# Performance work log

Measured on AMD Instinct MI355X. Metric: run time of the kernel, lower is better.

The kernel has to match this reference:

```python
import jax, jax.numpy as jnp
import numpy as np

B, S, HID = 2, 2048, 4096
NH, NKV, D = 32, 8, 128
GROUPS = NH // NKV  # 4 query heads per KV head
THETA = 10000.0
MAX_SEQ = 4096


def _rope_tables():
    half = D // 2
    inv_freq = 1.0 / (THETA ** (np.arange(half, dtype=np.float32) / half))
    t = np.arange(MAX_SEQ, dtype=np.float32)
    freqs = np.outer(t, inv_freq)  # [MAX_SEQ, D//2]
    return jnp.asarray(np.cos(freqs)), jnp.asarray(np.sin(freqs))

ROPE_COS, ROPE_SIN = _rope_tables()


def _apply_rope(x, cos, sin):
    # x: [B, S, H, D]; cos/sin: [S, D//2]; half-split (NeoX) rotation as in _apply_rope_inline
    half = x.shape[-1] // 2
    x0, x1 = x[..., :half], x[..., half:]
    c = cos[None, :, None, :]
    s = sin[None, :, None, :]
    return jnp.concatenate([x0 * c - x1 * s, x0 * s + x1 * c], axis=-1)


def setup_inputs() -> dict:
    key = jax.random.key(0)
    ks = jax.random.split(key, 5)
    wscale = 1.0 / np.sqrt(HID).astype(np.float32)  # keep activations O(1)
    return {
        "x": jax.random.normal(ks[0], (B, S, HID), dtype=jnp.float32),
        "positions": jnp.arange(S, dtype=jnp.int32),
        "w_q": jax.random.normal(ks[1], (NH * D, HID), dtype=jnp.float32) * wscale,
        "w_k": jax.random.normal(ks[2], (NKV * D, HID), dtype=jnp.float32) * wscale,
        "w_v": jax.random.normal(ks[3], (NKV * D, HID), dtype=jnp.float32) * wscale,
        "w_o": jax.random.normal(ks[4], (HID, NH * D), dtype=jnp.float32) * wscale,
    }


def reference(x, positions, w_q, w_k, w_v, w_o):
    cos = ROPE_COS[positions]  # [S, D//2]
    sin = ROPE_SIN[positions]
    # Separate Q/K/V projections (no bias), as in the training forward()
    q = (x @ w_q.T).reshape(B, S, NH, D)
    k = (x @ w_k.T).reshape(B, S, NKV, D)
    v = (x @ w_v.T).reshape(B, S, NKV, D)
    q = _apply_rope(q, cos, sin)
    k = _apply_rope(k, cos, sin)
    # [B, H, S, D] layout
    q = q.transpose(0, 2, 1, 3)
    k = k.transpose(0, 2, 1, 3)
    v = v.transpose(0, 2, 1, 3)
    # GQA: group query heads over shared KV heads instead of repeating K/V
    qg = q.reshape(B, NKV, GROUPS, S, D)
    scale = 1.0 / jnp.sqrt(jnp.float32(D))
    scores = jnp.einsum("bkgqd,bkmd->bkgqm", qg, k) * scale  # [B, NKV, G, Sq, Skv]
    causal = jnp.tril(jnp.ones((S, S), dtype=bool))
    scores = jnp.where(causal[None, None, None], scores, jnp.float32(-jnp.inf))
    probs = jax.nn.softmax(scores, axis=-1)
    ctx = jnp.einsum("bkgqm,bkmd->bkgqd", probs, v)  # [B, NKV, G, S, D]
    ctx = ctx.reshape(B, NH, S, D).transpose(0, 2, 1, 3).reshape(B, S, NH * D)
    return ctx @ w_o.T
```

## Files before the change

### kernel.cpp

```cpp
#include <hip/hip_runtime.h>
#include <math.h>

typedef short s16x8 __attribute__((ext_vector_type(8)));
typedef float f32x4 __attribute__((ext_vector_type(4)));
typedef unsigned u32x4 __attribute__((ext_vector_type(4)));
typedef unsigned short u16;

#define S_LEN 2048
#define HID_DIM 4096
#define NH_Q 32
#define NKV_H 8
#define DHEAD 128

__device__ __forceinline__ u16 f2bf(float f) {
  unsigned u = __builtin_bit_cast(unsigned, f);
  u += 0x7fffu + ((u >> 16) & 1u);
  return (u16)(u >> 16);
}

__device__ __forceinline__ void gload16(const u16* g, u16* l) {
  __builtin_amdgcn_global_load_lds(
      (const __attribute__((address_space(1))) void*)g,
      (__attribute__((address_space(3))) void*)l, 16, 0, 0);
}

__global__ void cvt_kernel(const float* __restrict__ in, u16* __restrict__ out, int n4) {
  int stride = gridDim.x * blockDim.x;
  for (int i = blockIdx.x * blockDim.x + threadIdx.x; i < n4; i += stride) {
    float4 f = ((const float4*)in)[i];
    uint2 o;
    o.x = (unsigned)f2bf(f.x) | ((unsigned)f2bf(f.y) << 16);
    o.y = (unsigned)f2bf(f.z) | ((unsigned)f2bf(f.w) << 16);
    ((uint2*)out)[i] = o;
  }
}

__global__ void cvt_all_kernel(const float* __restrict__ x, const float* __restrict__ wq,
                               const float* __restrict__ wk, const float* __restrict__ wv,
                               const float* __restrict__ wo, u16* __restrict__ x_bf,
                               u16* __restrict__ wqkv_bf, u16* __restrict__ wo_bf,
                               const int* __restrict__ positions, float* __restrict__ cos_t,
                               float* __restrict__ sin_t, int with_wo) {
  const int R0 = 4194304, R1 = 8388608, R2 = 9437184, R3 = 10485760, R4 = 14680064;
  const int cvt_end = with_wo ? R4 : R3;
  const int rope_units = 32768;
  const int total = cvt_end + rope_units;
  const int stride = gridDim.x * blockDim.x;
  for (int i = blockIdx.x * blockDim.x + threadIdx.x; i < total; i += stride) {
    if (i < cvt_end) {
      const float* src;
      u16* dst;
      int off;
      if (i < R0)      { src = x;  dst = x_bf;               off = i; }
      else if (i < R1) { src = wq; dst = wqkv_bf;            off = i - R0; }
      else if (i < R2) { src = wk; dst = wqkv_bf + 16777216; off = i - R1; }
      else if (i < R3) { src = wv; dst = wqkv_bf + 20971520; off = i - R2; }
      else             { src = wo; dst = wo_bf;              off = i - R3; }
      float4 f = ((const float4*)src)[off];
      uint2 o;
      o.x = (unsigned)f2bf(f.x) | ((unsigned)f2bf(f.y) << 16);
      o.y = (unsigned)f2bf(f.z) | ((unsigned)f2bf(f.w) << 16);
      ((uint2*)dst)[off] = o;
    } else {
      int base = (i - cvt_end) * 4;
#pragma unroll
      for (int e = 0; e < 4; ++e) {
        int idx = base + e;
        int s = idx >> 6, j = idx & 63;
        float pos = (float)positions[s];
        float inv = expf(-(float)j * (9.210340371976184f / 64.0f));
        float sv, cv;
        sincosf(pos * inv, &sv, &cv);
        cos_t[idx] = cv;
        sin_t[idx] = sv;
      }
    }
  }
}

__global__ void rope_table_kernel(const int* __restrict__ positions,
                                  float* __restrict__ cos_t, float* __restrict__ sin_t) {
  int idx = blockIdx.x * 256 + threadIdx.x;
  if (idx >= S_LEN * 64) return;
  int s = idx >> 6, j = idx & 63;
  float pos = (float)positions[s];
  float inv = expf(-(float)j * (9.210340371976184f / 64.0f));
  float sv, cv;
  sincosf(pos * inv, &sv, &cv);
  cos_t[idx] = cv;
  sin_t[idx] = sv;
}

template<int EPI>
__global__ __launch_bounds__(512, 2) void gemmp_kernel(
    const u16* __restrict__ A, const u16* __restrict__ B,
    void* __restrict__ outp, int M, int N, int K,
    const float* __restrict__ cos_t, const float* __restrict__ sin_t) {
  __shared__ u16 LDS[73728];
  const int t = threadIdx.x;
  const int wave = t >> 6, lane = t & 63;
  const int l15 = lane & 15, lhi = lane >> 4;
  const int wr = wave >> 2, wc = wave & 3;
  const int gx = gridDim.x;
  const int nwg = gx * gridDim.y;
  const int id = blockIdx.y * gx + blockIdx.x;
  const int swz = (id & 7) * (nwg >> 3) + (id >> 3);
  const int bm = (swz / gx) * 128, bn = (swz % gx) * 256;

  const int sw = l15 & 7;
  int aoff[4][2], boff[2][2];
#pragma unroll
  for (int q = 0; q < 4; ++q)
#pragma unroll
    for (int ks = 0; ks < 2; ++ks)
      aoff[q][ks] = wr * 4096 + (q * 16 + l15) * 64 + (((ks << 2) + lhi) ^ sw) * 8;
#pragma unroll
  for (int f = 0; f < 2; ++f)
#pragma unroll
    for (int ks = 0; ks < 2; ++ks)
      boff[f][ks] = (f * 64 + wc * 16 + l15) * 64 + (((ks << 2) + lhi) ^ sw) * 8;

  const int lr1 = t >> 3;
  const int cs1 = ((t & 7) ^ (lr1 & 7)) * 8;
  const int ldsw = wave * 512;

  const f32x4 fz = {0.f, 0.f, 0.f, 0.f};
  f32x4 acc[4][4];
#pragma unroll
  for (int mf = 0; mf < 4; ++mf)
#pragma unroll
    for (int nf = 0; nf < 4; ++nf) acc[mf][nf] = fz;

  auto stageA = [&](int tile, int buf) {
    const size_t kb = (size_t)tile * 64;
    gload16(A + (size_t)(bm + lr1) * K + kb + cs1, &LDS[buf * 8192 + ldsw]);
    gload16(A + (size_t)(bm + 64 + lr1) * K + kb + cs1, &LDS[buf * 8192 + 4096 + ldsw]);
  };
  auto stageB = [&](int tile, int h, int buf) {
    const size_t kb = (size_t)tile * 64;
    gload16(B + (size_t)(bn + h * 128 + lr1) * K + kb + cs1,
            &LDS[24576 + buf * 16384 + h * 8192 + ldsw]);
    gload16(B + (size_t)(bn + h * 128 + 64 + lr1) * K + kb + cs1,
            &LDS[24576 + buf * 16384 + h * 8192 + 4096 + ldsw]);
  };

  s16x8 afr0[4][2], afr1[4][2];
  s16x8 bfr00[2][2], bfr01[2][2];
  s16x8 bfr10[2][2], bfr11[2][2];

#define READ_TILE(SET, BUF)                                                \
  do {                                                                     \
    const int _b = (BUF);                                                  \
    const int _ba = _b * 8192;                                             \
    _Pragma("unroll") for (int q = 0; q < 4; ++q)                          \
      _Pragma("unroll") for (int ks = 0; ks < 2; ++ks)                     \
        afr##SET[q][ks] = *(const s16x8*)&LDS[_ba + aoff[q][ks]];          \
    const int _b0 = 24576 + _b * 16384;                                    \
    _Pragma("unroll") for (int f = 0; f < 2; ++f)                          \
      _Pragma("unroll") for (int ks = 0; ks < 2; ++ks)                     \
        bfr0##SET[f][ks] = *(const s16x8*)&LDS[_b0 + boff[f][ks]];         \
    const int _b1 = _b0 + 8192;                                            \
    _Pragma("unroll") for (int f = 0; f < 2; ++f)                          \
      _Pragma("unroll") for (int ks = 0; ks < 2; ++ks)                     \
        bfr1##SET[f][ks] = *(const s16x8*)&LDS[_b1 + boff[f][ks]];         \
  } while (0)

#define MFMA_HALF(SET, NFH, BH)                                            \
  do {                                                                     \
    __builtin_amdgcn_s_setprio(1);                                         \
    _Pragma("unroll") for (int q = 0; q < 4; ++q)                          \
      _Pragma("unroll") for (int f = 0; f < 2; ++f)                        \
        _Pragma("unroll") for (int ks = 0; ks < 2; ++ks)                   \
          acc[q][(NFH)*2 + f] = __builtin_amdgcn_mfma_f32_16x16x32_bf16(   \
              afr##SET[q][ks], bfr##BH##SET[f][ks], acc[q][(NFH)*2 + f],   \
              0, 0, 0);                                                    \
    __builtin_amdgcn_s_setprio(0);                                         \
  } while (0)

#define TILE_BODY(SET, OSET, TT)                                           \
  do {                                                                     \
    const int _tt = (TT);                                                  \
    const bool _s2 = _tt + 2 < nt;                                         \
    if (_s2) { stageA(_tt + 2, nx2); stageB(_tt + 2, 0, nx2); }            \
    asm volatile("s_waitcnt lgkmcnt(0)" ::: "memory");                     \
    __builtin_amdgcn_sched_barrier(0);                                     \
    MFMA_HALF(SET, 0, 0);                                                  \
    if (_s2) stageB(_tt + 2, 1, nx2);                                      \
    if (_tt + 1 < nt) {                                                    \
      if (_s2) { asm volatile("s_waitcnt vmcnt(6)" ::: "memory"); }        \
      else     { asm volatile("s_waitcnt vmcnt(0)" ::: "memory"); }        \
      __builtin_amdgcn_sched_barrier(0);                                   \
      __builtin_amdgcn_s_barrier();                                        \
      __builtin_amdgcn_sched_barrier(0);                                   \
      READ_TILE(OSET, nxt1);                                               \
    }                                                                      \
    MFMA_HALF(SET, 1, 1);                                                  \
    nxt1 = nx2;                                                            \
    nx2 = (nx2 == 2) ? 0 : nx2 + 1;                                        \
  } while (0)

  const int nt = K >> 6;
  stageA(0, 0); stageB(0, 0, 0); stageB(0, 1, 0);
  stageA(1, 1); stageB(1, 0, 1); stageB(1, 1, 1);
  asm volatile("s_waitcnt vmcnt(6)" ::: "memory");
  __builtin_amdgcn_sched_barrier(0);
  __builtin_amdgcn_s_barrier();
  __builtin_amdgcn_sched_barrier(0);
  READ_TILE(0, 0);

  int nxt1 = 1, nx2 = 2;
  for (int tt = 0; tt < nt; tt += 2) {
    TILE_BODY(0, 1, tt);
    TILE_BODY(1, 0, tt + 1);
  }
#undef TILE_BODY
#undef MFMA_HALF
#undef READ_TILE

  if constexpr (EPI == 0) {
    float* C = (float*)outp;
#pragma unroll
    for (int mf = 0; mf < 4; ++mf) {
      int rb = bm + wr * 64 + mf * 16 + lhi * 4;
#pragma unroll
      for (int nfi = 0; nfi < 4; ++nfi) {
        int col = bn + wc * 16 + (nfi & 1) * 64 + (nfi >> 1) * 128 + l15;
#pragma unroll
        for (int i = 0; i < 4; ++i) C[(size_t)(rb + i) * N + col] = acc[mf][nfi][i];
      }
    }
  } else {
    u16* qp = (u16*)outp;
    u16* kp = qp + 16777216;
    u16* vp = kp + 4194304;
    if (bn < 5120) {
      const bool isQ = bn < 4096;
      u16* O = isQ ? qp : kp;
      const int hb = isQ ? (bn >> 7) : ((bn - 4096) >> 7);
      const int Hh = isQ ? NH_Q : NKV_H;
      const int j = wc * 16 + l15;
#pragma unroll
      for (int mf = 0; mf < 4; ++mf) {
        int rb = bm + wr * 64 + mf * 16 + lhi * 4;
#pragma unroll
        for (int p = 0; p < 2; ++p) {
          int head = hb + p;
#pragma unroll
          for (int i = 0; i < 4; ++i) {
            int m = rb + i;
            int b = m >> 11, srw = m & 2047;
            float c = cos_t[srw * 64 + j];
            float s = sin_t[srw * 64 + j];
            float x0 = acc[mf][2 * p][i];
            float x1 = acc[mf][2 * p + 1][i];
            size_t base = ((size_t)(b * Hh + head) * S_LEN + srw) * DHEAD;
            O[base + j] = f2bf(x0 * c - x1 * s);
            O[base + j + 64] = f2bf(x0 * s + x1 * c);
          }
        }
      }
    } else {
#pragma unroll
      for (int mf = 0; mf < 4; ++mf) {
        int rb = bm + wr * 64 + mf * 16 + lhi * 4;
#pragma unroll
        for (int nfi = 0; nfi < 4; ++nfi) {
          int colrel = bn - 5120 + wc * 16 + (nfi & 1) * 64 + (nfi >> 1) * 128 + l15;
          int head = colrel >> 7, d = colrel & 127;
#pragma unroll
          for (int i = 0; i < 4; ++i) {
            int m = rb + i;
            int b = m >> 11, srw = m & 2047;
            vp[((size_t)(b * NKV_H + head) * DHEAD + d) * S_LEN + srw] = f2bf(acc[mf][nfi][i]);
          }
        }
      }
    }
  }
}

template<int EPI, bool ABF16, bool BBF16>
__global__ __launch_bounds__(256) void gemm_kernel(
    const void* __restrict__ Aptr, const void* __restrict__ Bptr,
    void* __restrict__ outp, void* __restrict__ outp2, int M, int N, int K,
    const float* __restrict__ cos_t, const float* __restrict__ sin_t, int Hh) {
  __shared__ u16 As[128][72];
  __shared__ u16 Bs[128][72];
  const int t = threadIdx.x;
  const int wave = t >> 6, lane = t & 63;
  const int l15 = lane & 15, lhi = lane >> 4;
  const int gx = gridDim.x;
  const int nwg = gx * gridDim.y;
  const int id = blockIdx.y * gx + blockIdx.x;
  const int swz = (id & 7) * (nwg >> 3) + (id >> 3);
  const int bm = (swz / gx) * 128, bn = (swz % gx) * 128;

  const f32x4 fz = {0.f, 0.f, 0.f, 0.f};
  f32x4 acc[2][8];
#pragma unroll
  for (int a0 = 0; a0 < 2; ++a0)
#pragma unroll
    for (int b0 = 0; b0 < 8; ++b0) acc[a0][b0] = fz;

  for (int kt = 0; kt < K; kt += 64) {
    __syncthreads();
    if (ABF16) {
      const u16* A = (const u16*)Aptr;
#pragma unroll
      for (int p = 0; p < 4; ++p) {
        int row = p * 32 + (t >> 3), kc = (t & 7) * 8;
        *(s16x8*)&As[row][kc] = *(const s16x8*)(A + (size_t)(bm + row) * K + kt + kc);
      }
    } else {
      const float* A = (const float*)Aptr;
#pragma unroll
      for (int p = 0; p < 8; ++p) {
        int row = p * 16 + (t >> 4), kc = (t & 15) * 4;
        float4 f = *(const float4*)(A + (size_t)(bm + row) * K + kt + kc);
        unsigned* dst = (unsigned*)&As[row][kc];
        dst[0] = (unsigned)f2bf(f.x) | ((unsigned)f2bf(f.y) << 16);
        dst[1] = (unsigned)f2bf(f.z) | ((unsigned)f2bf(f.w) << 16);
      }
    }
    if (BBF16) {
      const u16* Bw = (const u16*)Bptr;
#pragma unroll
      for (int p = 0; p < 4; ++p) {
        int row = p * 32 + (t >> 3), kc = (t & 7) * 8;
        *(s16x8*)&Bs[row][kc] = *(const s16x8*)(Bw + (size_t)(bn + row) * K + kt + kc);
      }
    } else {
      const float* Bw = (const float*)Bptr;
#pragma unroll
      for (int p = 0; p < 8; ++p) {
        int row = p * 16 + (t >> 4), kc = (t & 15) * 4;
        float4 f = *(const float4*)(Bw + (size_t)(bn + row) * K + kt + kc);
        unsigned* dst = (unsigned*)&Bs[row][kc];
        dst[0] = (unsigned)f2bf(f.x) | ((unsigned)f2bf(f.y) << 16);
        dst[1] = (unsigned)f2bf(f.z) | ((unsigned)f2bf(f.w) << 16);
      }
    }
    __syncthreads();
#pragma unroll
    for (int ks = 0; ks < 2; ++ks) {
      s16x8 bfr[8];
#pragma unroll
      for (int nf = 0; nf < 8; ++nf)
        bfr[nf] = *(const s16x8*)&Bs[nf * 16 + l15][ks * 32 + lhi * 8];
#pragma unroll
      for (int mf = 0; mf < 2; ++mf) {
        s16x8 a = *(const s16x8*)&As[wave * 32 + mf * 16 + l15][ks * 32 + lhi * 8];
#pragma unroll
        for (int nf = 0; nf < 8; ++nf)
          acc[mf][nf] = __builtin_amdgcn_mfma_f32_16x16x32_bf16(a, bfr[nf], acc[mf][nf], 0, 0, 0);
      }
    }
  }

  if (EPI == 0) {
    float* C = (float*)outp;
#pragma unroll
    for (int mf = 0; mf < 2; ++mf)
#pragma unroll
      for (int nf = 0; nf < 8; ++nf) {
        int col = bn + nf * 16 + l15;
        int rb = bm + wave * 32 + mf * 16 + lhi * 4;
#pragma unroll
        for (int i = 0; i < 4; ++i) C[(size_t)(rb + i) * N + col] = acc[mf][nf][i];
      }
  } else if (EPI == 2) {
    u16* O = (u16*)outp;
    int h = bn >> 7;
#pragma unroll
    for (int mf = 0; mf < 2; ++mf)
#pragma unroll
      for (int nf = 0; nf < 4; ++nf) {
        int j = nf * 16 + l15;
        int rb = bm + wave * 32 + mf * 16 + lhi * 4;
#pragma unroll
        for (int i = 0; i < 4; ++i) {
          int m = rb + i;
          int b = m >> 11, srow = m & 2047;
          float c = cos_t[srow * 64 + j];
          float s = sin_t[srow * 64 + j];
          float x0 = acc[mf][nf][i];
          float x1 = acc[mf][nf + 4][i];
          size_t base = ((size_t)(b * Hh + h) * S_LEN + srow) * DHEAD;
          O[base + j] = f2bf(x0 * c - x1 * s);
          O[base + j + 64] = f2bf(x0 * s + x1 * c);
        }
      }
  } else {
    u16* O = (u16*)outp;
#pragma unroll
    for (int mf = 0; mf < 2; ++mf)
#pragma unroll
      for (int nf = 0; nf < 8; ++nf) {
        int col = bn + nf * 16 + l15;
        int h = col >> 7, d = col & 127;
        int rb = bm + wave * 32 + mf * 16 + lhi * 4;
#pragma unroll
        for (int i = 0; i < 4; ++i) {
          int m = rb + i;
          int b = m >> 11, srow = m & 2047;
          O[((size_t)(b * Hh + h) * DHEAD + d) * S_LEN + srow] = f2bf(acc[mf][nf][i]);
        }
      }
  }
}

#define KIDX(r, c) (((r) * 128 + (c)) ^ (((r) & 7) << 3))
#define VIDX(d, kv) (((d) * 64 + (kv)) ^ (((d) & 7) << 3))
__global__ __launch_bounds__(512) void attn_kernel(
    const u16* __restrict__ q, const u16* __restrict__ k, const u16* __restrict__ vt,
    u16* __restrict__ ctx) {
  __shared__ u16 Ks[64 * 128];
  __shared__ u16 Vts[128 * 64];

  const int t = threadIdx.x;
  const int wave = t >> 6, lane = t & 63;
  const int l15 = lane & 15, lhi = lane >> 4;
  const int pi = blockIdx.x, h = blockIdx.y, b = blockIdx.z;
  const int kvh = h >> 2;
  const int qsub[2] = {pi, 15 - pi};
  const int ntiles = 32 - 2 * pi;

  const u16* qb = q + ((size_t)(b * NH_Q + h)) * S_LEN * DHEAD;
  const u16* kb = k + ((size_t)(b * NKV_H + kvh)) * S_LEN * DHEAD;
  const u16* vtb = vt + ((size_t)(b * NKV_H + kvh)) * DHEAD * S_LEN;

  s16x8 qf[2][4];
#pragma unroll
  for (int s = 0; s < 2; ++s)
#pragma unroll
    for (int ks = 0; ks < 4; ++ks)
      qf[s][ks] = *(const s16x8*)(qb + (size_t)(qsub[s] * 128 + wave * 16 + l15) * DHEAD +
                                  ks * 32 + lhi * 8);

  const f32x4 fz = {0.f, 0.f, 0.f, 0.f};
  f32x4 acc[2][8];
#pragma unroll
  for (int s = 0; s < 2; ++s)
#pragma unroll
    for (int i = 0; i < 8; ++i) acc[s][i] = fz;
  float mrow[2] = {-INFINITY, -INFINITY};
  float lsum[2] = {0.f, 0.f};

  const float scale = 0.08838834764831845f;

  const int sl0 = l15 | (((2 * lhi) & 3) << 4);
  const int sl1 = sl0 | 16;
  const bool hisel = (lhi & 2) != 0;

  const int krow = t >> 3, kd0 = (t & 7) * 16;
  const int vrow = t >> 2, vk0 = (t & 3) * 16;
  s16x8 kr0, kr1, vr0, vr1;
  {
    const u16* p = kb + (size_t)krow * DHEAD + kd0;
    kr0 = *(const s16x8*)p;
    kr1 = *(const s16x8*)(p + 8);
    const u16* pv = vtb + (size_t)vrow * S_LEN + vk0;
    vr0 = *(const s16x8*)pv;
    vr1 = *(const s16x8*)(pv + 8);
  }

  for (int tt = 0; tt < ntiles; ++tt) {
    __syncthreads();
    *(s16x8*)&Ks[KIDX(krow, kd0)] = kr0;
    *(s16x8*)&Ks[KIDX(krow, kd0 + 8)] = kr1;
    *(s16x8*)&Vts[VIDX(vrow, vk0)] = vr0;
    *(s16x8*)&Vts[VIDX(vrow, vk0 + 8)] = vr1;
    __syncthreads();
    if (tt + 1 < ntiles) {
      const u16* p = kb + (size_t)((tt + 1) * 64 + krow) * DHEAD + kd0;
      kr0 = *(const s16x8*)p;
      kr1 = *(const s16x8*)(p + 8);
      const u16* pv = vtb + (size_t)vrow * S_LEN + (tt + 1) * 64 + vk0;
      vr0 = *(const s16x8*)pv;
      vr1 = *(const s16x8*)(pv + 8);
    }

    const int kc_base = tt * 64;
#pragma unroll
    for (int s = 0; s < 2; ++s) {
      const int wmin = qsub[s] * 128 + wave * 16;
      if (kc_base > wmin + 15) continue;
      f32x4 sacc[4];
#pragma unroll
      for (int i = 0; i < 4; ++i) sacc[i] = fz;
      __builtin_amdgcn_s_setprio(1);
#pragma unroll
      for (int ks = 0; ks < 4; ++ks) {
#pragma unroll
        for (int nf = 0; nf < 4; ++nf) {
          s16x8 kf = *(const s16x8*)&Ks[KIDX(nf * 16 + l15, ks * 32 + lhi * 8)];
          sacc[nf] = __builtin_amdgcn_mfma_f32_16x16x32_bf16(kf, qf[s][ks], sacc[nf], 0, 0, 0);
        }
      }
      __builtin_amdgcn_s_setprio(0);

      const int qg = wmin + l15;
      float pmax = -INFINITY;
      if (kc_base + 63 > wmin) {
#pragma unroll
        for (int nf = 0; nf < 4; ++nf)
#pragma unroll
          for (int i = 0; i < 4; ++i) {
            int kv = kc_base + nf * 16 + lhi * 4 + i;
            float sv = sacc[nf][i] * scale;
            sv = (kv <= qg) ? sv : -INFINITY;
            sacc[nf][i] = sv;
            pmax = fmaxf(pmax, sv);
          }
      } else {
#pragma unroll
        for (int nf = 0; nf < 4; ++nf)
#pragma unroll
          for (int i = 0; i < 4; ++i) {
            float sv = sacc[nf][i] * scale;
            sacc[nf][i] = sv;
            pmax = fmaxf(pmax, sv);
          }
      }
      pmax = fmaxf(pmax, __shfl_xor(pmax, 16, 64));
      pmax = fmaxf(pmax, __shfl_xor(pmax, 32, 64));

      if (!__all(pmax <= mrow[s] + 8.0f)) {
        float mnew = fmaxf(mrow[s], pmax);
        float alpha = __expf(mrow[s] - mnew);
        mrow[s] = mnew;
        lsum[s] *= alpha;
#pragma unroll
        for (int i = 0; i < 4; ++i) {
          float al = __shfl(alpha, (lane & 48) | (lhi * 4 + i), 64);
#pragma unroll
          for (int df = 0; df < 8; ++df) acc[s][df][i] *= al;
        }
      }

      float rsum = 0.f;
      unsigned pk[4][2];
#pragma unroll
      for (int nf = 0; nf < 4; ++nf) {
        float p0 = __expf(sacc[nf][0] - mrow[s]);
        float p1 = __expf(sacc[nf][1] - mrow[s]);
        float p2 = __expf(sacc[nf][2] - mrow[s]);
        float p3 = __expf(sacc[nf][3] - mrow[s]);
        rsum += (p0 + p1) + (p2 + p3);
        pk[nf][0] = (unsigned)f2bf(p0) | ((unsigned)f2bf(p1) << 16);
        pk[nf][1] = (unsigned)f2bf(p2) | ((unsigned)f2bf(p3) << 16);
      }
      rsum += __shfl_xor(rsum, 16, 64);
      rsum += __shfl_xor(rsum, 32, 64);
      lsum[s] += rsum;

      s16x8 pa[2];
#pragma unroll
      for (int ph = 0; ph < 2; ++ph) {
        unsigned lo0 = __shfl((int)pk[2 * ph][0], sl0, 64);
        unsigned hi0 = __shfl((int)pk[2 * ph + 1][0], sl0, 64);
        unsigned lo1 = __shfl((int)pk[2 * ph][1], sl0, 64);
        unsigned hi1 = __shfl((int)pk[2 * ph + 1][1], sl0, 64);
        unsigned lo2 = __shfl((int)pk[2 * ph][0], sl1, 64);
        unsigned hi2 = __shfl((int)pk[2 * ph + 1][0], sl1, 64);
        unsigned lo3 = __shfl((int)pk[2 * ph][1], sl1, 64);
        unsigned hi3 = __shfl((int)pk[2 * ph + 1][1], sl1, 64);
        u32x4 w;
        w[0] = hisel ? hi0 : lo0;
        w[1] = hisel ? hi1 : lo1;
        w[2] = hisel ? hi2 : lo2;
        w[3] = hisel ? hi3 : lo3;
        pa[ph] = __builtin_bit_cast(s16x8, w);
      }

      __builtin_amdgcn_s_setprio(1);
#pragma unroll
      for (int ph = 0; ph < 2; ++ph) {
#pragma unroll
        for (int df = 0; df < 8; ++df) {
          s16x8 bb = *(const s16x8*)&Vts[VIDX(df * 16 + l15, ph * 32 + lhi * 8)];
          acc[s][df] = __builtin_amdgcn_mfma_f32_16x16x32_bf16(pa[ph], bb, acc[s][df], 0, 0, 0);
        }
      }
      __builtin_amdgcn_s_setprio(0);
    }
  }

#pragma unroll
  for (int s = 0; s < 2; ++s) {
    float rl = 1.0f / lsum[s];
#pragma unroll
    for (int i = 0; i < 4; ++i) {
      float rli = __shfl(rl, (lane & 48) | (lhi * 4 + i), 64);
      int m = b * S_LEN + qsub[s] * 128 + wave * 16 + lhi * 4 + i;
#pragma unroll
      for (int df = 0; df < 8; ++df) {
        int col = h * DHEAD + df * 16 + l15;
        ctx[(size_t)m * (NH_Q * DHEAD) + col] = f2bf(acc[s][df][i] * rli);
      }
    }
  }
}

extern "C" void kernel_launch(void* const* d_in, const int* in_sizes, int n_in,
                              void* d_out, int out_size, void* d_ws, size_t ws_size,
                              hipStream_t stream) {
  const float* x = (const float*)d_in[0];
  const int* positions = (const int*)d_in[1];
  const float* wq = (const float*)d_in[2];
  const float* wk = (const float*)d_in[3];
  const float* wv = (const float*)d_in[4];
  const float* wo = (const float*)d_in[5];
  float* out = (float*)d_out;

  char* ws = (char*)d_ws;
  const size_t MB1 = 1048576;
  const size_t SZ_X = 33554432;
  const size_t SZ_WQKV = 50331648;
  const size_t SZ_WO = 33554432;
  const size_t SZ_Q = 33554432;
  const size_t SZ_WK = 8388608;
  const size_t NEED_FULL = MB1 + SZ_X + SZ_WQKV + SZ_Q + 2 * SZ_WK;
  const size_t NEED_WO = NEED_FULL + SZ_WO;

  float* cos_t = (float*)ws;
  float* sin_t = (float*)(ws + MB1 / 2);

  if (ws_size >= NEED_WO) {
    char* p = ws + MB1;
    u16* x_bf = (u16*)p;    p += SZ_X;
    u16* wqkv_bf = (u16*)p; p += SZ_WQKV;
    u16* wo_bf = (u16*)p;   p += SZ_WO;
    u16* q_ws = (u16*)p;    p += SZ_Q;
    u16* k_ws = (u16*)p;    p += SZ_WK;
    u16* v_ws = (u16*)p;    p += SZ_WK;
    u16* ctx_ws = x_bf;

    cvt_all_kernel<<<2048, 256, 0, stream>>>(x, wq, wk, wv, wo, x_bf, wqkv_bf, wo_bf,
                                             positions, cos_t, sin_t, 1);
    gemmp_kernel<5><<<dim3(24, 32), 512, 0, stream>>>(
        x_bf, wqkv_bf, q_ws, 4096, 6144, 4096, cos_t, sin_t);
    attn_kernel<<<dim3(8, 32, 2), 512, 0, stream>>>(q_ws, k_ws, v_ws, ctx_ws);
    gemmp_kernel<0><<<dim3(16, 32), 512, 0, stream>>>(
        ctx_ws, wo_bf, out, 4096, 4096, 4096, nullptr, nullptr);
  } else if (ws_size >= NEED_FULL) {
    char* p = ws + MB1;
    u16* x_bf = (u16*)p;    p += SZ_X;
    u16* wqkv_bf = (u16*)p; p += SZ_WQKV;
    u16* q_ws = (u16*)p;    p += SZ_Q;
    u16* k_ws = (u16*)p;    p += SZ_WK;
    u16* v_ws = (u16*)p;    p += SZ_WK;
    u16* ctx_ws = x_bf;

    cvt_all_kernel<<<2048, 256, 0, stream>>>(x, wq, wk, wv, nullptr, x_bf, wqkv_bf, nullptr,
                                             positions, cos_t, sin_t, 0);
    gemmp_kernel<5><<<dim3(24, 32), 512, 0, stream>>>(
        x_bf, wqkv_bf, q_ws, 4096, 6144, 4096, cos_t, sin_t);
    cvt_kernel<<<2048, 256, 0, stream>>>(wo, wqkv_bf, 4194304);
    attn_kernel<<<dim3(8, 32, 2), 512, 0, stream>>>(q_ws, k_ws, v_ws, ctx_ws);
    gemmp_kernel<0><<<dim3(16, 32), 512, 0, stream>>>(
        ctx_ws, wqkv_bf, out, 4096, 4096, 4096, nullptr, nullptr);
  } else {
    u16* q_ws = (u16*)(ws + MB1);
    u16* k_ws = (u16*)(ws + MB1 + SZ_Q);
    u16* v_ws = (u16*)(ws + MB1 + SZ_Q + SZ_WK);
    u16* ctx_ws = (u16*)(ws + MB1 + SZ_Q + 2 * SZ_WK);

    rope_table_kernel<<<512, 256, 0, stream>>>(positions, cos_t, sin_t);
    gemm_kernel<2, false, false><<<dim3(32, 32), 256, 0, stream>>>(
        x, wq, q_ws, nullptr, 4096, 4096, 4096, cos_t, sin_t, NH_Q);
    gemm_kernel<2, false, false><<<dim3(8, 32), 256, 0, stream>>>(
        x, wk, k_ws, nullptr, 4096, 1024, 4096, cos_t, sin_t, NKV_H);
    gemm_kernel<4, false, false><<<dim3(8, 32), 256, 0, stream>>>(
        x, wv, v_ws, nullptr, 4096, 1024, 4096, nullptr, nullptr, NKV_H);
    attn_kernel<<<dim3(8, 32, 2), 512, 0, stream>>>(q_ws, k_ws, v_ws, ctx_ws);
    gemm_kernel<0, true, false><<<dim3(32, 32), 256, 0, stream>>>(
        ctx_ws, wo, out, nullptr, 4096, 4096, 4096, nullptr, nullptr, 0);
  }
}
```

Before: 532.9 us.

## Rework projection GEMM to 4-wave blocks with 64x128 warp tiles and K=32 stages

```diff
diff --git a/kernel.cpp b/kernel.cpp
--- a/kernel.cpp
+++ b/kernel.cpp
@@ -92,130 +92,97 @@
 }
 
 template<int EPI>
-__global__ __launch_bounds__(512, 2) void gemmp_kernel(
+__global__ __launch_bounds__(256, 2) void gemmp_kernel(
     const u16* __restrict__ A, const u16* __restrict__ B,
     void* __restrict__ outp, int M, int N, int K,
     const float* __restrict__ cos_t, const float* __restrict__ sin_t) {
-  __shared__ u16 LDS[73728];
+  __shared__ u16 LDS[36864];
   const int t = threadIdx.x;
   const int wave = t >> 6, lane = t & 63;
   const int l15 = lane & 15, lhi = lane >> 4;
-  const int wr = wave >> 2, wc = wave & 3;
+  const int wr = wave >> 1, wc = wave & 1;
   const int gx = gridDim.x;
   const int nwg = gx * gridDim.y;
   const int id = blockIdx.y * gx + blockIdx.x;
   const int swz = (id & 7) * (nwg >> 3) + (id >> 3);
   const int bm = (swz / gx) * 128, bn = (swz % gx) * 256;
 
-  const int sw = l15 & 7;
-  int aoff[4][2], boff[2][2];
-#pragma unroll
-  for (int q = 0; q < 4; ++q)
-#pragma unroll
-    for (int ks = 0; ks < 2; ++ks)
-      aoff[q][ks] = wr * 4096 + (q * 16 + l15) * 64 + (((ks << 2) + lhi) ^ sw) * 8;
-#pragma unroll
-  for (int f = 0; f < 2; ++f)
-#pragma unroll
-    for (int ks = 0; ks < 2; ++ks)
-      boff[f][ks] = (f * 64 + wc * 16 + l15) * 64 + (((ks << 2) + lhi) ^ sw) * 8;
-
-  const int lr1 = t >> 3;
-  const int cs1 = ((t & 7) ^ (lr1 & 7)) * 8;
-  const int ldsw = wave * 512;
+  const int sw = (l15 >> 1) & 3;
+  int aoff[4], boff[8];
+#pragma unroll
+  for (int mf = 0; mf < 4; ++mf)
+    aoff[mf] = (wr * 64 + mf * 16 + l15) * 32 + ((lhi ^ sw) << 3);
+#pragma unroll
+  for (int nf = 0; nf < 8; ++nf)
+    boff[nf] = (wc * 16 + nf * 32 + l15) * 32 + ((lhi ^ sw) << 3);
+
+  const int r0 = t >> 2;
+  const int cs = (((t & 3) ^ ((t >> 3) & 3)) << 3);
 
   const f32x4 fz = {0.f, 0.f, 0.f, 0.f};
-  f32x4 acc[4][4];
+  f32x4 acc[4][8];
 #pragma unroll
   for (int mf = 0; mf < 4; ++mf)
 #pragma unroll
-    for (int nf = 0; nf < 4; ++nf) acc[mf][nf] = fz;
+    for (int nf = 0; nf < 8; ++nf) acc[mf][nf] = fz;
 
   auto stageA = [&](int tile, int buf) {
-    const size_t kb = (size_t)tile * 64;
-    gload16(A + (size_t)(bm + lr1) * K + kb + cs1, &LDS[buf * 8192 + ldsw]);
-    gload16(A + (size_t)(bm + 64 + lr1) * K + kb + cs1, &LDS[buf * 8192 + 4096 + ldsw]);
+    const size_t kb = (size_t)tile * 32;
+    const u16* s0 = A + (size_t)(bm + r0) * K + kb + cs;
+    u16* d = &LDS[buf * 4096 + (wave << 9)];
+    gload16(s0, d);
+    gload16(s0 + (size_t)64 * K, d + 2048);
   };
-  auto stageB = [&](int tile, int h, int buf) {
-    const size_t kb = (size_t)tile * 64;
-    gload16(B + (size_t)(bn + h * 128 + lr1) * K + kb + cs1,
-            &LDS[24576 + buf * 16384 + h * 8192 + ldsw]);
-    gload16(B + (size_t)(bn + h * 128 + 64 + lr1) * K + kb + cs1,
-            &LDS[24576 + buf * 16384 + h * 8192 + 4096 + ldsw]);
+  auto stageB = [&](int tile, int buf) {
+    const size_t kb = (size_t)tile * 32;
+    const u16* s0 = B + (size_t)(bn + r0) * K + kb + cs;
+    u16* d = &LDS[12288 + buf * 8192 + (wave << 9)];
+    gload16(s0, d);
+    gload16(s0 + (size_t)64 * K, d + 2048);
+    gload16(s0 + (size_t)128 * K, d + 4096);
+    gload16(s0 + (size_t)192 * K, d + 6144);
   };
 
-  s16x8 afr0[4][2], afr1[4][2];
-  s16x8 bfr00[2][2], bfr01[2][2];
-  s16x8 bfr10[2][2], bfr11[2][2];
-
-#define READ_TILE(SET, BUF)                                                \
-  do {                                                                     \
-    const int _b = (BUF);                                                  \
-    const int _ba = _b * 8192;                                             \
-    _Pragma("unroll") for (int q = 0; q < 4; ++q)                          \
-      _Pragma("unroll") for (int ks = 0; ks < 2; ++ks)                     \
-        afr##SET[q][ks] = *(const s16x8*)&LDS[_ba + aoff[q][ks]];          \
-    const int _b0 = 24576 + _b * 16384;                                    \
-    _Pragma("unroll") for (int f = 0; f < 2; ++f)                          \
-      _Pragma("unroll") for (int ks = 0; ks < 2; ++ks)                     \
-        bfr0##SET[f][ks] = *(const s16x8*)&LDS[_b0 + boff[f][ks]];         \
-    const int _b1 = _b0 + 8192;                                            \
-    _Pragma("unroll") for (int f = 0; f < 2; ++f)                          \
-      _Pragma("unroll") for (int ks = 0; ks < 2; ++ks)                     \
-        bfr1##SET[f][ks] = *(const s16x8*)&LDS[_b1 + boff[f][ks]];         \
-  } while (0)
-
-#define MFMA_HALF(SET, NFH, BH)                                            \
-  do {                                                                     \
-    __builtin_amdgcn_s_setprio(1);                                         \
-    _Pragma("unroll") for (int q = 0; q < 4; ++q)                          \
-      _Pragma("unroll") for (int f = 0; f < 2; ++f)                        \
-        _Pragma("unroll") for (int ks = 0; ks < 2; ++ks)                   \
-          acc[q][(NFH)*2 + f] = __builtin_amdgcn_mfma_f32_16x16x32_bf16(   \
-              afr##SET[q][ks], bfr##BH##SET[f][ks], acc[q][(NFH)*2 + f],   \
-              0, 0, 0);                                                    \
-    __builtin_amdgcn_s_setprio(0);                                         \
-  } while (0)
-
-#define TILE_BODY(SET, OSET, TT)                                           \
-  do {                                                                     \
-    const int _tt = (TT);                                                  \
-    const bool _s2 = _tt + 2 < nt;                                         \
-    if (_s2) { stageA(_tt + 2, nx2); stageB(_tt + 2, 0, nx2); }            \
-    asm volatile("s_waitcnt lgkmcnt(0)" ::: "memory");                     \
-    __builtin_amdgcn_sched_barrier(0);                                     \
-    MFMA_HALF(SET, 0, 0);                                                  \
-    if (_s2) stageB(_tt + 2, 1, nx2);                                      \
-    if (_tt + 1 < nt) {                                                    \
-      if (_s2) { asm volatile("s_waitcnt vmcnt(6)" ::: "memory"); }        \
-      else     { asm volatile("s_waitcnt vmcnt(0)" ::: "memory"); }        \
-      __builtin_amdgcn_sched_barrier(0);                                   \
-      __builtin_amdgcn_s_barrier();                                        \
-      __builtin_amdgcn_sched_barrier(0);                                   \
-      READ_TILE(OSET, nxt1);                                               \
-    }                                                                      \
-    MFMA_HALF(SET, 1, 1);                                                  \
-    nxt1 = nx2;                                                            \
-    nx2 = (nx2 == 2) ? 0 : nx2 + 1;                                        \
-  } while (0)
-
-  const int nt = K >> 6;
-  stageA(0, 0); stageB(0, 0, 0); stageB(0, 1, 0);
-  stageA(1, 1); stageB(1, 0, 1); stageB(1, 1, 1);
-  asm volatile("s_waitcnt vmcnt(6)" ::: "memory");
-  __builtin_amdgcn_sched_barrier(0);
-  __builtin_amdgcn_s_barrier();
-  __builtin_amdgcn_sched_barrier(0);
-  READ_TILE(0, 0);
-
-  int nxt1 = 1, nx2 = 2;
-  for (int tt = 0; tt < nt; tt += 2) {
-    TILE_BODY(0, 1, tt);
-    TILE_BODY(1, 0, tt + 1);
-  }
-#undef TILE_BODY
-#undef MFMA_HALF
-#undef READ_TILE
+  const int nt = K >> 5;
+  stageA(0, 0); stageB(0, 0);
+  stageA(1, 1); stageB(1, 1);
+
+  int cur = 0, nx2 = 2;
+  s16x8 afr[4], bfr[8];
+  for (int tt = 0; tt < nt; ++tt) {
+    if (tt + 2 < nt) {
+      stageA(tt + 2, nx2); stageB(tt + 2, nx2);
+      asm volatile("s_waitcnt vmcnt(12)" ::: "memory");
+    } else if (tt + 1 < nt) {
+      asm volatile("s_waitcnt vmcnt(6)" ::: "memory");
+    } else {
+      asm volatile("s_waitcnt vmcnt(0)" ::: "memory");
+    }
+    __builtin_amdgcn_sched_barrier(0);
+    __builtin_amdgcn_s_barrier();
+    __builtin_amdgcn_sched_barrier(0);
+
+    const int ab = cur * 4096;
+    const int bb = 12288 + cur * 8192;
+#pragma unroll
+    for (int mf = 0; mf < 4; ++mf) afr[mf] = *(const s16x8*)&LDS[ab + aoff[mf]];
+#pragma unroll
+    for (int nf = 0; nf < 8; ++nf) bfr[nf] = *(const s16x8*)&LDS[bb + boff[nf]];
+    asm volatile("s_waitcnt lgkmcnt(0)" ::: "memory");
+    __builtin_amdgcn_sched_barrier(0);
+    __builtin_amdgcn_s_barrier();
+
+    __builtin_amdgcn_s_setprio(1);
+#pragma unroll
+    for (int mf = 0; mf < 4; ++mf)
+#pragma unroll
+      for (int nf = 0; nf < 8; ++nf)
+        acc[mf][nf] = __builtin_amdgcn_mfma_f32_16x16x32_bf16(afr[mf], bfr[nf], acc[mf][nf], 0, 0, 0);
+    __builtin_amdgcn_s_setprio(0);
+
+    cur = (cur == 2) ? 0 : cur + 1;
+    nx2 = (nx2 == 2) ? 0 : nx2 + 1;
+  }
 
   if constexpr (EPI == 0) {
     float* C = (float*)outp;
@@ -223,8 +190,8 @@
     for (int mf = 0; mf < 4; ++mf) {
       int rb = bm + wr * 64 + mf * 16 + lhi * 4;
 #pragma unroll
-      for (int nfi = 0; nfi < 4; ++nfi) {
-        int col = bn + wc * 16 + (nfi & 1) * 64 + (nfi >> 1) * 128 + l15;
+      for (int nfi = 0; nfi < 8; ++nfi) {
+        int col = bn + wc * 16 + nfi * 32 + l15;
 #pragma unroll
         for (int i = 0; i < 4; ++i) C[(size_t)(rb + i) * N + col] = acc[mf][nfi][i];
       }
@@ -238,7 +205,6 @@
       u16* O = isQ ? qp : kp;
       const int hb = isQ ? (bn >> 7) : ((bn - 4096) >> 7);
       const int Hh = isQ ? NH_Q : NKV_H;
-      const int j = wc * 16 + l15;
 #pragma unroll
       for (int mf = 0; mf < 4; ++mf) {
         int rb = bm + wr * 64 + mf * 16 + lhi * 4;
@@ -246,16 +212,20 @@
         for (int p = 0; p < 2; ++p) {
           int head = hb + p;
 #pragma unroll
-          for (int i = 0; i < 4; ++i) {
-            int m = rb + i;
-            int b = m >> 11, srw = m & 2047;
-            float c = cos_t[srw * 64 + j];
-            float s = sin_t[srw * 64 + j];
-            float x0 = acc[mf][2 * p][i];
-            float x1 = acc[mf][2 * p + 1][i];
-            size_t base = ((size_t)(b * Hh + head) * S_LEN + srw) * DHEAD;
-            O[base + j] = f2bf(x0 * c - x1 * s);
-            O[base + j + 64] = f2bf(x0 * s + x1 * c);
+          for (int q01 = 0; q01 < 2; ++q01) {
+            int j = wc * 16 + q01 * 32 + l15;
+#pragma unroll
+            for (int i = 0; i < 4; ++i) {
+              int m = rb + i;
+              int b = m >> 11, srw = m & 2047;
+              float c = cos_t[srw * 64 + j];
+              float s = sin_t[srw * 64 + j];
+              float x0 = acc[mf][p * 4 + q01][i];
+              float x1 = acc[mf][p * 4 + q01 + 2][i];
+              size_t base = ((size_t)(b * Hh + head) * S_LEN + srw) * DHEAD;
+              O[base + j] = f2bf(x0 * c - x1 * s);
+              O[base + j + 64] = f2bf(x0 * s + x1 * c);
+            }
           }
         }
       }
@@ -264,8 +234,8 @@
       for (int mf = 0; mf < 4; ++mf) {
         int rb = bm + wr * 64 + mf * 16 + lhi * 4;
 #pragma unroll
-        for (int nfi = 0; nfi < 4; ++nfi) {
-          int colrel = bn - 5120 + wc * 16 + (nfi & 1) * 64 + (nfi >> 1) * 128 + l15;
+        for (int nfi = 0; nfi < 8; ++nfi) {
+          int colrel = bn - 5120 + wc * 16 + nfi * 32 + l15;
           int head = colrel >> 7, d = colrel & 127;
 #pragma unroll
           for (int i = 0; i < 4; ++i) {
@@ -638,10 +608,10 @@
 
     cvt_all_kernel<<<2048, 256, 0, stream>>>(x, wq, wk, wv, wo, x_bf, wqkv_bf, wo_bf,
                                              positions, cos_t, sin_t, 1);
-    gemmp_kernel<5><<<dim3(24, 32), 512, 0, stream>>>(
+    gemmp_kernel<5><<<dim3(24, 32), 256, 0, stream>>>(
         x_bf, wqkv_bf, q_ws, 4096, 6144, 4096, cos_t, sin_t);
     attn_kernel<<<dim3(8, 32, 2), 512, 0, stream>>>(q_ws, k_ws, v_ws, ctx_ws);
-    gemmp_kernel<0><<<dim3(16, 32), 512, 0, stream>>>(
+    gemmp_kernel<0><<<dim3(16, 32), 256, 0, stream>>>(
         ctx_ws, wo_bf, out, 4096, 4096, 4096, nullptr, nullptr);
   } else if (ws_size >= NEED_FULL) {
     char* p = ws + MB1;
@@ -654,11 +624,11 @@
 
     cvt_all_kernel<<<2048, 256, 0, stream>>>(x, wq, wk, wv, nullptr, x_bf, wqkv_bf, nullptr,
                                              positions, cos_t, sin_t, 0);
-    gemmp_kernel<5><<<dim3(24, 32), 512, 0, stream>>>(
+    gemmp_kernel<5><<<dim3(24, 32), 256, 0, stream>>>(
         x_bf, wqkv_bf, q_ws, 4096, 6144, 4096, cos_t, sin_t);
     cvt_kernel<<<2048, 256, 0, stream>>>(wo, wqkv_bf, 4194304);
     attn_kernel<<<dim3(8, 32, 2), 512, 0, stream>>>(q_ws, k_ws, v_ws, ctx_ws);
-    gemmp_kernel<0><<<dim3(16, 32), 512, 0, stream>>>(
+    gemmp_kernel<0><<<dim3(16, 32), 256, 0, stream>>>(
         ctx_ws, wqkv_bf, out, 4096, 4096, 4096, nullptr, nullptr);
   } else {
     u16* q_ws = (u16*)(ws + MB1);
```

Measured after the change: 567.8 us. 6.6% more time.

## Add dedicated 256x256-tile output projection GEMM kernel with K=32 triple buffering

Applied to the files above, without the earlier changes.

```diff
diff --git a/kernel.cpp b/kernel.cpp
--- a/kernel.cpp
+++ b/kernel.cpp
@@ -217,64 +217,173 @@
 #undef MFMA_HALF
 #undef READ_TILE
 
-  if constexpr (EPI == 0) {
-    float* C = (float*)outp;
+  u16* qp = (u16*)outp;
+  u16* kp = qp + 16777216;
+  u16* vp = kp + 4194304;
+  if (bn < 5120) {
+    const bool isQ = bn < 4096;
+    u16* O = isQ ? qp : kp;
+    const int hb = isQ ? (bn >> 7) : ((bn - 4096) >> 7);
+    const int Hh = isQ ? NH_Q : NKV_H;
+    const int j = wc * 16 + l15;
 #pragma unroll
     for (int mf = 0; mf < 4; ++mf) {
       int rb = bm + wr * 64 + mf * 16 + lhi * 4;
 #pragma unroll
+      for (int p = 0; p < 2; ++p) {
+        int head = hb + p;
+#pragma unroll
+        for (int i = 0; i < 4; ++i) {
+          int m = rb + i;
+          int b = m >> 11, srw = m & 2047;
+          float c = cos_t[srw * 64 + j];
+          float s = sin_t[srw * 64 + j];
+          float x0 = acc[mf][2 * p][i];
+          float x1 = acc[mf][2 * p + 1][i];
+          size_t base = ((size_t)(b * Hh + head) * S_LEN + srw) * DHEAD;
+          O[base + j] = f2bf(x0 * c - x1 * s);
+          O[base + j + 64] = f2bf(x0 * s + x1 * c);
+        }
+      }
+    }
+  } else {
+#pragma unroll
+    for (int mf = 0; mf < 4; ++mf) {
+      int rb = bm + wr * 64 + mf * 16 + lhi * 4;
+#pragma unroll
       for (int nfi = 0; nfi < 4; ++nfi) {
-        int col = bn + wc * 16 + (nfi & 1) * 64 + (nfi >> 1) * 128 + l15;
-#pragma unroll
-        for (int i = 0; i < 4; ++i) C[(size_t)(rb + i) * N + col] = acc[mf][nfi][i];
-      }
-    }
-  } else {
-    u16* qp = (u16*)outp;
-    u16* kp = qp + 16777216;
-    u16* vp = kp + 4194304;
-    if (bn < 5120) {
-      const bool isQ = bn < 4096;
-      u16* O = isQ ? qp : kp;
-      const int hb = isQ ? (bn >> 7) : ((bn - 4096) >> 7);
-      const int Hh = isQ ? NH_Q : NKV_H;
-      const int j = wc * 16 + l15;
-#pragma unroll
-      for (int mf = 0; mf < 4; ++mf) {
-        int rb = bm + wr * 64 + mf * 16 + lhi * 4;
-#pragma unroll
-        for (int p = 0; p < 2; ++p) {
-          int head = hb + p;
-#pragma unroll
-          for (int i = 0; i < 4; ++i) {
-            int m = rb + i;
-            int b = m >> 11, srw = m & 2047;
-            float c = cos_t[srw * 64 + j];
-            float s = sin_t[srw * 64 + j];
-            float x0 = acc[mf][2 * p][i];
-            float x1 = acc[mf][2 * p + 1][i];
-            size_t base = ((size_t)(b * Hh + head) * S_LEN + srw) * DHEAD;
-            O[base + j] = f2bf(x0 * c - x1 * s);
-            O[base + j + 64] = f2bf(x0 * s + x1 * c);
-          }
+        int colrel = bn - 5120 + wc * 16 + (nfi & 1) * 64 + (nfi >> 1) * 128 + l15;
+        int head = colrel >> 7, d = colrel & 127;
+#pragma unroll
+        for (int i = 0; i < 4; ++i) {
+          int m = rb + i;
+          int b = m >> 11, srw = m & 2047;
+          vp[((size_t)(b * NKV_H + head) * DHEAD + d) * S_LEN + srw] = f2bf(acc[mf][nfi][i]);
         }
       }
-    } else {
-#pragma unroll
-      for (int mf = 0; mf < 4; ++mf) {
-        int rb = bm + wr * 64 + mf * 16 + lhi * 4;
-#pragma unroll
-        for (int nfi = 0; nfi < 4; ++nfi) {
-          int colrel = bn - 5120 + wc * 16 + (nfi & 1) * 64 + (nfi >> 1) * 128 + l15;
-          int head = colrel >> 7, d = colrel & 127;
-#pragma unroll
-          for (int i = 0; i < 4; ++i) {
-            int m = rb + i;
-            int b = m >> 11, srw = m & 2047;
-            vp[((size_t)(b * NKV_H + head) * DHEAD + d) * S_LEN + srw] = f2bf(acc[mf][nfi][i]);
-          }
-        }
-      }
+    }
+  }
+}
+
+__global__ __launch_bounds__(512, 1) void gemmo_kernel(
+    const u16* __restrict__ A, const u16* __restrict__ B,
+    float* __restrict__ C, int M, int N, int K) {
+  __shared__ u16 LDS[49152];
+  const int t = threadIdx.x;
+  const int wave = t >> 6, lane = t & 63;
+  const int l15 = lane & 15, lhi = lane >> 4;
+  const int wr = wave >> 1, wc = wave & 1;
+  const int gx = gridDim.x;
+  const int nwg = gx * gridDim.y;
+  const int id = blockIdx.y * gx + blockIdx.x;
+  const int swz = (id & 7) * (nwg >> 3) + (id >> 3);
+  const int bm = (swz / gx) * 256, bn = (swz % gx) * 256;
+
+  const int sw = (l15 >> 1) & 3;
+  int aoff[4], boff[8];
+#pragma unroll
+  for (int mf = 0; mf < 4; ++mf)
+    aoff[mf] = (wr * 64 + mf * 16 + l15) * 32 + ((lhi ^ sw) << 3);
+#pragma unroll
+  for (int nf = 0; nf < 8; ++nf)
+    boff[nf] = (wc * 128 + nf * 16 + l15) * 32 + ((lhi ^ sw) << 3);
+
+  const int r0 = t >> 2;
+  const int cs = (((t & 3) ^ ((t >> 3) & 3)) << 3);
+
+  const f32x4 fz = {0.f, 0.f, 0.f, 0.f};
+  f32x4 acc[4][8];
+#pragma unroll
+  for (int mf = 0; mf < 4; ++mf)
+#pragma unroll
+    for (int nf = 0; nf < 8; ++nf) acc[mf][nf] = fz;
+
+  auto stageA = [&](int tile, int buf) {
+    const size_t kb = (size_t)tile * 32;
+    const u16* s0 = A + (size_t)(bm + r0) * K + kb + cs;
+    u16* d = &LDS[buf * 8192 + (wave << 9)];
+    gload16(s0, d);
+    gload16(s0 + (size_t)128 * K, d + 4096);
+  };
+  auto stageB = [&](int tile, int buf) {
+    const size_t kb = (size_t)tile * 32;
+    const u16* s0 = B + (size_t)(bn + r0) * K + kb + cs;
+    u16* d = &LDS[24576 + buf * 8192 + (wave << 9)];
+    gload16(s0, d);
+    gload16(s0 + (size_t)128 * K, d + 4096);
+  };
+
+  s16x8 afr0[4], afr1[4], bfr0[8], bfr1[8];
+
+#define READ_TILE(SET, BUF)                                                \
+  do {                                                                     \
+    const int _ab = (BUF) * 8192;                                          \
+    const int _bb = 24576 + (BUF) * 8192;                                  \
+    _Pragma("unroll") for (int mf = 0; mf < 4; ++mf)                       \
+      afr##SET[mf] = *(const s16x8*)&LDS[_ab + aoff[mf]];                  \
+    _Pragma("unroll") for (int nf = 0; nf < 8; ++nf)                       \
+      bfr##SET[nf] = *(const s16x8*)&LDS[_bb + boff[nf]];                  \
+  } while (0)
+
+#define MFMA_HALF(SET, H)                                                  \
+  do {                                                                     \
+    __builtin_amdgcn_s_setprio(1);                                         \
+    _Pragma("unroll") for (int mf = 0; mf < 4; ++mf)                       \
+      _Pragma("unroll") for (int nf = 0; nf < 4; ++nf)                     \
+        acc[mf][(H)*4 + nf] = __builtin_amdgcn_mfma_f32_16x16x32_bf16(     \
+            afr##SET[mf], bfr##SET[(H)*4 + nf], acc[mf][(H)*4 + nf],       \
+            0, 0, 0);                                                      \
+    __builtin_amdgcn_s_setprio(0);                                         \
+  } while (0)
+
+#define TILE_BODY(SET, OSET, TT)                                           \
+  do {                                                                     \
+    const int _tt = (TT);                                                  \
+    const bool _s2 = _tt + 2 < nt;                                         \
+    if (_s2) stageA(_tt + 2, nx2);                                         \
+    asm volatile("s_waitcnt lgkmcnt(0)" ::: "memory");                     \
+    __builtin_amdgcn_sched_barrier(0);                                     \
+    MFMA_HALF(SET, 0);                                                     \
+    if (_s2) stageB(_tt + 2, nx2);                                         \
+    if (_tt + 1 < nt) {                                                    \
+      if (_s2) { asm volatile("s_waitcnt vmcnt(4)" ::: "memory"); }        \
+      else     { asm volatile("s_waitcnt vmcnt(0)" ::: "memory"); }        \
+      __builtin_amdgcn_sched_barrier(0);                                   \
+      __builtin_amdgcn_s_barrier();                                        \
+      __builtin_amdgcn_sched_barrier(0);                                   \
+      READ_TILE(OSET, nxt1);                                               \
+    }                                                                      \
+    MFMA_HALF(SET, 1);                                                     \
+    nxt1 = nx2;                                                            \
+    nx2 = (nx2 == 2) ? 0 : nx2 + 1;                                        \
+  } while (0)
+
+  const int nt = K >> 5;
+  stageA(0, 0); stageB(0, 0);
+  stageA(1, 1); stageB(1, 1);
+  asm volatile("s_waitcnt vmcnt(4)" ::: "memory");
+  __builtin_amdgcn_sched_barrier(0);
+  __builtin_amdgcn_s_barrier();
+  __builtin_amdgcn_sched_barrier(0);
+  READ_TILE(0, 0);
+
+  int nxt1 = 1, nx2 = 2;
+  for (int tt = 0; tt < nt; tt += 2) {
+    TILE_BODY(0, 1, tt);
+    TILE_BODY(1, 0, tt + 1);
+  }
+#undef TILE_BODY
+#undef MFMA_HALF
+#undef READ_TILE
+
+#pragma unroll
+  for (int mf = 0; mf < 4; ++mf) {
+    int rb = bm + wr * 64 + mf * 16 + lhi * 4;
+#pragma unroll
+    for (int nf = 0; nf < 8; ++nf) {
+      int col = bn + wc * 128 + nf * 16 + l15;
+#pragma unroll
+      for (int i = 0; i < 4; ++i) C[(size_t)(rb + i) * N + col] = acc[mf][nf][i];
     }
   }
 }
@@ -641,8 +750,8 @@
     gemmp_kernel<5><<<dim3(24, 32), 512, 0, stream>>>(
         x_bf, wqkv_bf, q_ws, 4096, 6144, 4096, cos_t, sin_t);
     attn_kernel<<<dim3(8, 32, 2), 512, 0, stream>>>(q_ws, k_ws, v_ws, ctx_ws);
-    gemmp_kernel<0><<<dim3(16, 32), 512, 0, stream>>>(
-        ctx_ws, wo_bf, out, 4096, 4096, 4096, nullptr, nullptr);
+    gemmo_kernel<<<dim3(16, 16), 512, 0, stream>>>(
+        ctx_ws, wo_bf, out, 4096, 4096, 4096);
   } else if (ws_size >= NEED_FULL) {
     char* p = ws + MB1;
     u16* x_bf = (u16*)p;    p += SZ_X;
@@ -658,8 +767,8 @@
         x_bf, wqkv_bf, q_ws, 4096, 6144, 4096, cos_t, sin_t);
     cvt_kernel<<<2048, 256, 0, stream>>>(wo, wqkv_bf, 4194304);
     attn_kernel<<<dim3(8, 32, 2), 512, 0, stream>>>(q_ws, k_ws, v_ws, ctx_ws);
-    gemmp_kernel<0><<<dim3(16, 32), 512, 0, stream>>>(
-        ctx_ws, wqkv_bf, out, 4096, 4096, 4096, nullptr, nullptr);
+    gemmo_kernel<<<dim3(16, 16), 512, 0, stream>>>(
+        ctx_ws, wqkv_bf, out, 4096, 4096, 4096);
   } else {
     u16* q_ws = (u16*)(ws + MB1);
     u16* k_ws = (u16*)(ws + MB1 + SZ_Q);
```

New measurement: 522.5 us. About the same (-2.0%).
